# Performance work log

Hardware: AMD Instinct MI355X
Metric: run time of the kernel (lower is better)

The kernel has to match this reference:

```python
import jax, jax.numpy as jnp
import numpy as np

K = 7                 # kernel_size = inhibition_kernel.shape[3]
PAD = 3               # hardcoded ReflectionPad2d((3,3,3,3))
MEMBRANE_DECAY = 0.99


def setup_inputs() -> dict:
    key = jax.random.key(0)
    k1, k2 = jax.random.split(key)
    B, C, H, W = 16, 16, 64, 64
    # spikes are binary events; sparse-ish activity
    in_spikes = (jax.random.uniform(k1, (B, C, H, W)) < 0.1).astype(jnp.float32)
    # weights: (out_h, out_w, C_in, k, k, C_out), init randn * 1/(k*k)
    weights = jax.random.normal(k2, (H, W, C, K, K, C), dtype=jnp.float32) * (1.0 / (K * K))
    membrane = jnp.ones((B, C, H, W), dtype=jnp.float32)
    return {"in_spikes": in_spikes, "weights": weights, "membrane": membrane}


def reference(in_spikes, weights, membrane):
    B, C, H, W = in_spikes.shape
    # ReflectionPad2d(3) on both spatial dims
    padded = jnp.pad(in_spikes, ((0, 0), (0, 0), (PAD, PAD), (PAD, PAD)), mode="reflect")
    # Extract all kxk patches (stride 1): fixed 49 shifted views -> (B, C, K, K, H, W)
    patches = jnp.stack(
        [padded[:, :, ki:ki + H, kj:kj + W] for ki in range(K) for kj in range(K)],
        axis=2,
    ).reshape(B, C, K, K, H, W)
    # Locally-connected (unshared weights) reduce over (c, ki, kj) per output location (i, j):
    # out[b, m, i, j] = sum_{c,x,y} patches[b, c, x, y, i, j] * weights[i, j, c, x, y, m]
    local = jnp.einsum("bcxyij,ijcxym->bmij", patches, weights)
    # LIF membrane/spike update
    mem = membrane * MEMBRANE_DECAY + local
    spike = (mem > 1).astype(in_spikes.dtype)
    mem = jnp.where(mem > 1, jnp.asarray(1.0, mem.dtype), mem)
    return spike, mem
```

## Files before the change

kernel.cpp:

```cpp
#include <hip/hip_runtime.h>

#define HW 64
#define KTOT 784
#define WPB_BYTES 50176u
#define W_TOTAL_BYTES (4096u * WPB_BYTES)
#define WEND (W_TOTAL_BYTES - 16u)

__device__ __forceinline__ void gl16(const void* g, void* l) {
    __builtin_amdgcn_global_load_lds(
        (const __attribute__((address_space(1))) unsigned int*)g,
        (__attribute__((address_space(3))) unsigned int*)l, 16, 0, 0);
}

#define FMA16(acc0, acc1, acc2, acc3, wv, sv)                                 \
    acc0.x += wv.x * sv.x; acc0.y += wv.x * sv.y;                             \
    acc0.z += wv.x * sv.z; acc0.w += wv.x * sv.w;                             \
    acc1.x += wv.y * sv.x; acc1.y += wv.y * sv.y;                             \
    acc1.z += wv.y * sv.z; acc1.w += wv.y * sv.w;                             \
    acc2.x += wv.z * sv.x; acc2.y += wv.z * sv.y;                             \
    acc2.z += wv.z * sv.z; acc2.w += wv.z * sv.w;                             \
    acc3.x += wv.w * sv.x; acc3.y += wv.w * sv.y;                             \
    acc3.z += wv.w * sv.z; acc3.w += wv.w * sv.w;

__global__ __launch_bounds__(256) void k_transpose(const float* __restrict__ in,
                                                   float* __restrict__ sT) {
    __shared__ float tile[16][66];
    const int c = blockIdx.x >> 6;
    const int h = blockIdx.x & 63;
    const int t = threadIdx.x;
    const int wid = t >> 6, l = t & 63;
#pragma unroll
    for (int p = 0; p < 4; ++p) {
        int b = p * 4 + wid;
        tile[b][l] = in[((b << 4) + c) * 4096 + (h << 6) + l];
    }
    __syncthreads();
    const int base = ((c << 6) | h) << 10;
#pragma unroll
    for (int p = 0; p < 4; ++p) {
        int idx = p * 256 + t;
        sT[base + idx] = tile[idx & 15][idx >> 4];
    }
}

__global__ __launch_bounds__(256) void k_lc(const float* __restrict__ weights,
                                            const float* __restrict__ sT,
                                            float* __restrict__ oc) {
    __shared__ __align__(16) float s_spk[12544];
    __shared__ __align__(16) float s_w[3][2048];

    const int tid = threadIdx.x;
    const int bid = blockIdx.x;
    const int i = bid >> 6, j = bid & 63;
    const int wid = tid >> 6, lane = tid & 63;
    const int kq = (lane >> 4) & 3;
    const int mq = (lane >> 2) & 3;
    const int bq = lane & 3;

    const char* wbase = (const char*)weights;
    const char* sbase = (const char*)sT;
    const unsigned wblk = (unsigned)bid * WPB_BYTES;

    for (int s = wid; s < 49; s += 4) {
        int k = s * 16 + (lane >> 2);
        int c = (k * 1338) >> 16;
        int xy = k - c * 49;
        int x = (xy * 37) >> 8;
        int y = xy - x * 7;
        int r = i + x - 3; r = r < 0 ? -r : r; r = r > 63 ? 126 - r : r;
        int q = j + y - 3; q = q < 0 ? -q : q; q = q > 63 ? 126 - q : q;
        unsigned off = (unsigned)(((c << 12) | (r << 6) | q) << 6)
                     + (unsigned)((lane & 3) << 4);
        gl16(sbase + off, (char*)s_spk + s * 1024);
    }
#pragma unroll
    for (int nn = 0; nn < 3; ++nn) {
#pragma unroll
        for (int L = 0; L < 2; ++L) {
            unsigned off = wblk + (unsigned)nn * 8192u
                         + (unsigned)((L * 4 + wid) << 10) + (unsigned)(lane << 4);
            off = off > WEND ? WEND : off;
            gl16(wbase + off, (char*)&s_w[nn][0] + ((L * 4 + wid) << 10));
        }
    }
    asm volatile("s_waitcnt vmcnt(0)" ::: "memory");
    __builtin_amdgcn_s_barrier();

    float4 acc0 = make_float4(0.f, 0.f, 0.f, 0.f);
    float4 acc1 = make_float4(0.f, 0.f, 0.f, 0.f);
    float4 acc2 = make_float4(0.f, 0.f, 0.f, 0.f);
    float4 acc3 = make_float4(0.f, 0.f, 0.f, 0.f);

    const int klb = wid * 32 + kq;
    int nb = 0;
    for (int n = 0; n < 6; ++n) {
        const float4* sp = (const float4*)s_spk + (((n << 7) + klb) << 2) + bq;
        const float4* wp = (const float4*)&s_w[nb][0] + (klb << 2) + mq;
#pragma unroll
        for (int t = 0; t < 8; ++t) {
            float4 sv = sp[t * 16];
            float4 wv = wp[t * 16];
            FMA16(acc0, acc1, acc2, acc3, wv, sv)
        }
        asm volatile("s_waitcnt lgkmcnt(0)" ::: "memory");
        __builtin_amdgcn_s_barrier();
        {
            const int nc = n + 3;
#pragma unroll
            for (int L = 0; L < 2; ++L) {
                unsigned off;
                if (nc <= 6) {
                    off = wblk + (unsigned)nc * 8192u
                        + (unsigned)((L * 4 + wid) << 10) + (unsigned)(lane << 4);
                    off = off > WEND ? WEND : off;
                } else {
                    off = WEND;
                }
                gl16(wbase + off, (char*)&s_w[nb][0] + ((L * 4 + wid) << 10));
            }
        }
        asm volatile("s_waitcnt vmcnt(4)" ::: "memory");
        __builtin_amdgcn_s_barrier();
        nb = nb + 1; if (nb == 3) nb = 0;
    }
    {
        const int klt = wid * 4 + kq;
        float4 sv = *((const float4*)s_spk + ((768 + klt) << 2) + bq);
        float4 wv = *((const float4*)&s_w[0][0] + (klt << 2) + mq);
        FMA16(acc0, acc1, acc2, acc3, wv, sv)
    }

    __syncthreads();
    float* scr = s_spk;
    {
        const int g = wid * 4 + kq;
        float4* scw = (float4*)scr;
        scw[(g * 16 + mq * 4 + 0) * 4 + bq] = acc0;
        scw[(g * 16 + mq * 4 + 1) * 4 + bq] = acc1;
        scw[(g * 16 + mq * 4 + 2) * 4 + bq] = acc2;
        scw[(g * 16 + mq * 4 + 3) * 4 + bq] = acc3;
    }
    __syncthreads();
    const int b = tid >> 4, mm = tid & 15;
    float sum = 0.f;
#pragma unroll
    for (int g = 0; g < 16; ++g) {
        sum += scr[g * 256 + mm * 16 + b];
    }
    oc[(size_t)bid * 256 + tid] = sum;
}

__global__ __launch_bounds__(256) void k_lif(const float* __restrict__ oc,
                                             const float* __restrict__ membrane,
                                             float* __restrict__ out) {
    __shared__ float tile[64][65];
    const int tb = blockIdx.x;
    const int ij0 = (tb >> 2) * 64;
    const int bm0 = (tb & 3) * 64;
    const int t = threadIdx.x;
    const int r0 = t >> 6;
    const int cl = t & 63;

#pragma unroll
    for (int p = 0; p < 16; ++p) {
        int ijl = p * 4 + r0;
        tile[ijl][cl] = oc[(size_t)(ij0 + ijl) * 256 + bm0 + cl];
    }
    __syncthreads();
#pragma unroll
    for (int p = 0; p < 16; ++p) {
        int bml = p * 4 + r0;
        int ijl = cl;
        float local = tile[ijl][bml];
        size_t idx = (size_t)(bm0 + bml) * 4096 + (ij0 + ijl);
        float memv = membrane[idx] * 0.99f + local;
        float spk = (memv > 1.0f) ? 1.0f : 0.0f;
        float mo = (memv > 1.0f) ? 1.0f : memv;
        out[idx] = spk;
        out[idx + 1048576] = mo;
    }
}

extern "C" void kernel_launch(void* const* d_in, const int* in_sizes, int n_in,
                              void* d_out, int out_size, void* d_ws, size_t ws_size,
                              hipStream_t stream) {
    const float* spikes = (const float*)d_in[0];
    const float* weights = (const float*)d_in[1];
    const float* membrane = (const float*)d_in[2];
    float* out = (float*)d_out;

    float* sT = (float*)d_ws;
    float* oc = (float*)d_ws + (1 << 20);

    k_transpose<<<1024, 256, 0, stream>>>(spikes, sT);
    k_lc<<<4096, 256, 0, stream>>>(weights, sT, oc);
    k_lif<<<256, 256, 0, stream>>>(oc, membrane, out);
}
```

Baseline: 302.7 us.

## Read weights directly from global memory instead of triple-buffered LDS staging

Drops the triple-buffered global-to-LDS weight pipeline, along with its barriers and waitcnt calls. Each thread now loads its weight float4s straight from global memory in one unrolled 49-step loop, and each wave takes a contiguous range of 196 k values. Spikes are still staged in LDS. This cuts LDS traffic and per-chunk synchronisation and frees LDS for more resident blocks. The cost is that weight streaming now relies on the compiler and cache to hide global latency, since there is no explicit prefetch.

```diff
diff --git a/kernel.cpp b/kernel.cpp
--- a/kernel.cpp
+++ b/kernel.cpp
@@ -1,10 +1,7 @@
 #include <hip/hip_runtime.h>
 
-#define HW 64
 #define KTOT 784
-#define WPB_BYTES 50176u
-#define W_TOTAL_BYTES (4096u * WPB_BYTES)
-#define WEND (W_TOTAL_BYTES - 16u)
+#define WPB 12544
 
 __device__ __forceinline__ void gl16(const void* g, void* l) {
     __builtin_amdgcn_global_load_lds(
@@ -47,7 +44,6 @@
                                             const float* __restrict__ sT,
                                             float* __restrict__ oc) {
     __shared__ __align__(16) float s_spk[12544];
-    __shared__ __align__(16) float s_w[3][2048];
 
     const int tid = threadIdx.x;
     const int bid = blockIdx.x;
@@ -57,10 +53,7 @@
     const int mq = (lane >> 2) & 3;
     const int bq = lane & 3;
 
-    const char* wbase = (const char*)weights;
     const char* sbase = (const char*)sT;
-    const unsigned wblk = (unsigned)bid * WPB_BYTES;
-
     for (int s = wid; s < 49; s += 4) {
         int k = s * 16 + (lane >> 2);
         int c = (k * 1338) >> 16;
@@ -73,60 +66,22 @@
                      + (unsigned)((lane & 3) << 4);
         gl16(sbase + off, (char*)s_spk + s * 1024);
     }
-#pragma unroll
-    for (int nn = 0; nn < 3; ++nn) {
-#pragma unroll
-        for (int L = 0; L < 2; ++L) {
-            unsigned off = wblk + (unsigned)nn * 8192u
-                         + (unsigned)((L * 4 + wid) << 10) + (unsigned)(lane << 4);
-            off = off > WEND ? WEND : off;
-            gl16(wbase + off, (char*)&s_w[nn][0] + ((L * 4 + wid) << 10));
-        }
-    }
     asm volatile("s_waitcnt vmcnt(0)" ::: "memory");
-    __builtin_amdgcn_s_barrier();
+    __syncthreads();
 
     float4 acc0 = make_float4(0.f, 0.f, 0.f, 0.f);
     float4 acc1 = make_float4(0.f, 0.f, 0.f, 0.f);
     float4 acc2 = make_float4(0.f, 0.f, 0.f, 0.f);
     float4 acc3 = make_float4(0.f, 0.f, 0.f, 0.f);
 
-    const int klb = wid * 32 + kq;
-    int nb = 0;
-    for (int n = 0; n < 6; ++n) {
-        const float4* sp = (const float4*)s_spk + (((n << 7) + klb) << 2) + bq;
-        const float4* wp = (const float4*)&s_w[nb][0] + (klb << 2) + mq;
-#pragma unroll
-        for (int t = 0; t < 8; ++t) {
-            float4 sv = sp[t * 16];
-            float4 wv = wp[t * 16];
-            FMA16(acc0, acc1, acc2, acc3, wv, sv)
-        }
-        asm volatile("s_waitcnt lgkmcnt(0)" ::: "memory");
-        __builtin_amdgcn_s_barrier();
-        {
-            const int nc = n + 3;
-#pragma unroll
-            for (int L = 0; L < 2; ++L) {
-                unsigned off;
-                if (nc <= 6) {
-                    off = wblk + (unsigned)nc * 8192u
-                        + (unsigned)((L * 4 + wid) << 10) + (unsigned)(lane << 4);
-                    off = off > WEND ? WEND : off;
-                } else {
-                    off = WEND;
-                }
-                gl16(wbase + off, (char*)&s_w[nb][0] + ((L * 4 + wid) << 10));
-            }
-        }
-        asm volatile("s_waitcnt vmcnt(4)" ::: "memory");
-        __builtin_amdgcn_s_barrier();
-        nb = nb + 1; if (nb == 3) nb = 0;
-    }
-    {
-        const int klt = wid * 4 + kq;
-        float4 sv = *((const float4*)s_spk + ((768 + klt) << 2) + bq);
-        float4 wv = *((const float4*)&s_w[0][0] + (klt << 2) + mq);
+    const int kbase = wid * 196 + kq;
+    const float4* sp = (const float4*)s_spk + kbase * 4 + bq;
+    const float4* wp = (const float4*)(weights + (size_t)bid * WPB) + kbase * 4 + mq;
+
+#pragma unroll 7
+    for (int t = 0; t < 49; ++t) {
+        float4 sv = sp[t * 16];
+        float4 wv = wp[t * 16];
         FMA16(acc0, acc1, acc2, acc3, wv, sv)
     }
 
```

After: 301.4 us. About the same (-0.5%).
